# Kernel optimization log

Hardware: AMD Instinct MI355X
Metric: run time of the kernel (lower is better)

Reference implementation:

```python
import jax, jax.numpy as jnp
import numpy as np

HIDDEN = 128
NUM_RADIAL = 16
NUM_DENSE = 3
OUT_DIM = 1
N_NODES = 50000
N_EDGES = 600000


def setup_inputs() -> dict:
    key = jax.random.key(0)
    ks = jax.random.split(key, 16)
    h = jax.random.normal(ks[0], (N_NODES, HIDDEN), dtype=jnp.float32)
    radial_basis = jax.random.normal(ks[1], (N_EDGES, NUM_RADIAL), dtype=jnp.float32)
    edge_index = jax.random.randint(ks[2], (2, N_EDGES), 0, N_NODES, dtype=jnp.int32)

    def lin(k, fan_in, fan_out):
        bound = 1.0 / np.sqrt(fan_in)
        kw, kb = jax.random.split(k)
        W = jax.random.uniform(kw, (fan_in, fan_out), minval=-bound, maxval=bound, dtype=jnp.float32)
        b = jax.random.uniform(kb, (fan_out,), minval=-bound, maxval=bound, dtype=jnp.float32)
        return W, b

    rW1, rb1 = lin(ks[3], NUM_RADIAL, HIDDEN)
    rW2, rb2 = lin(ks[4], HIDDEN, HIDDEN)
    dW, db = [], []
    for i in range(NUM_DENSE):
        W, b = lin(ks[5 + i], HIDDEN, HIDDEN)
        dW.append(W); db.append(b)
    oW, ob = lin(ks[10], HIDDEN, OUT_DIM)
    return {
        "h": h, "radial_basis": radial_basis, "edge_index": edge_index,
        "rW1": rW1, "rb1": rb1, "rW2": rW2, "rb2": rb2,
        "dW0": dW[0], "db0": db[0], "dW1": dW[1], "db1": db[1], "dW2": dW[2], "db2": db[2],
        "oW": oW, "ob": ob,
    }


def reference(h, radial_basis, edge_index, rW1, rb1, rW2, rb2,
              dW0, db0, dW1, db1, dW2, db2, oW, ob):
    src, dst = edge_index[0], edge_index[1]
    # radial_net: Linear -> SiLU -> Linear, output [n_edges, hidden]
    W = jax.nn.silu(radial_basis @ rW1 + rb1) @ rW2 + rb2
    # gather -> multiply -> scatter-add (message passing)
    h_edge = h[src] * W                      # [n_edges, hidden]
    x = jax.ops.segment_sum(h_edge, dst, num_segments=h.shape[0])  # [n_atoms, hidden]
    # dense layers
    for dw, dbias in ((dW0, db0), (dW1, db1), (dW2, db2)):
        x = jax.nn.silu(x @ dw + dbias)
    return x @ oW + ob                        # [n_atoms, output_dim]
```

## Files before the change

### kernel.cpp

```cpp
#include <hip/hip_runtime.h>

typedef short bf16x8 __attribute__((ext_vector_type(8)));
typedef float f32x4 __attribute__((ext_vector_type(4)));
typedef float f32x2 __attribute__((ext_vector_type(2)));
typedef unsigned int u32x4 __attribute__((ext_vector_type(4)));

__device__ __forceinline__ unsigned short f2bf(float f) {
  unsigned int u = __float_as_uint(f);
  u = (u + 0x7FFFu + ((u >> 16) & 1u)) >> 16;
  return (unsigned short)u;
}
__device__ __forceinline__ float bf2f(unsigned short u) {
  return __uint_as_float(((unsigned int)u) << 16);
}
__device__ __forceinline__ float silu_f(float v) {
  return v * (1.0f / (1.0f + __expf(-v)));
}
__device__ __forceinline__ unsigned int pkbf(float a, float b) {
  unsigned int r;
  asm("v_cvt_pk_bf16_f32 %0, %1, %2" : "=v"(r) : "v"(a), "v"(b));
  return r;
}
__device__ __forceinline__ void st2bf(char* base, int byA, int byB, float a, float b) {
  unsigned int p = pkbf(a, b);
  *(unsigned short*)(base + byA) = (unsigned short)p;
  *(unsigned short*)(base + byB) = (unsigned short)(p >> 16);
}

__global__ void k_prep(const float* __restrict__ rW1, const float* __restrict__ rb1,
                       const float* __restrict__ rW2, const float* __restrict__ dW0,
                       const float* __restrict__ dW1, const float* __restrict__ dW2,
                       unsigned short* __restrict__ wb, int* __restrict__ hist,
                       int nzero) {
  int i = blockIdx.x * blockDim.x + threadIdx.x;
  if (i < 4096) {
    int j = i & 7, lane = (i >> 3) & 63, nt = i >> 9;
    int k = (lane >> 4) * 8 + j, n = nt * 16 + (lane & 15);
    float v = (k < 16) ? rW1[k * 128 + n] : (k == 16 ? rb1[n] : 0.0f);
    wb[i] = f2bf(v);
  } else if (i < 4096 + 4 * 16384) {
    int i2 = i - 4096, buf = i2 >> 14, r = i2 & 16383;
    int j = r & 7, lane = (r >> 3) & 63, g = r >> 9, kc = g & 3, nt = g >> 2;
    int k = kc * 32 + (lane >> 4) * 8 + j, n = nt * 16 + (lane & 15);
    const float* W = (buf == 0) ? rW2 : (buf == 1) ? dW0 : (buf == 2) ? dW1 : dW2;
    wb[4096 + buf * 16384 + r] = f2bf(W[k * 128 + n]);
  } else if (i - 69632 < nzero) {
    hist[i - 69632] = 0;
  }
}

__global__ void k_hist(const int* __restrict__ ei, int* __restrict__ hist, int E) {
  int e = blockIdx.x * blockDim.x + threadIdx.x;
  if (e < E) atomicAdd(&hist[ei[E + e]], 1);
}

__global__ __launch_bounds__(1024) void k_scanA(const int* __restrict__ hist,
                                                int* __restrict__ part, int N) {
  __shared__ int red[1024];
  const int t = threadIdx.x;
  const int i = blockIdx.x * 1024 + t;
  red[t] = (i < N) ? hist[i] : 0;
  __syncthreads();
  for (int o = 512; o; o >>= 1) {
    if (t < o) red[t] += red[t + o];
    __syncthreads();
  }
  if (t == 0) part[blockIdx.x] = red[0];
}

__global__ __launch_bounds__(1024) void k_scanC(
    const int* __restrict__ hist, const int* __restrict__ part,
    int* __restrict__ row_start, int* __restrict__ bump, int N, int nb) {
  __shared__ int sh[1024];
  __shared__ int s_off;
  const int t = threadIdx.x;
  const int b = blockIdx.x;
  if (t < 64) {
    int p = (t < nb) ? part[t] : 0;
#pragma unroll
    for (int o = 1; o < 64; o <<= 1) {
      int u = __shfl_up(p, o);
      if (t >= o) p += u;
    }
    if (b == 0) {
      if (t == 0) s_off = 0;
    } else if (t == b - 1) {
      s_off = p;
    }
  }
  __syncthreads();
  const int i = b * 1024 + t;
  const int v = (i < N) ? hist[i] : 0;
  sh[t] = v;
  __syncthreads();
  for (int o = 1; o < 1024; o <<= 1) {
    int u = (t >= o) ? sh[t - o] : 0;
    __syncthreads();
    sh[t] += u;
    __syncthreads();
  }
  const int excl = s_off + sh[t] - v;
  if (i < N) {
    row_start[i] = excl;
    bump[i] = excl;
  } else if (i == N) {
    row_start[N] = excl;
  }
}

__global__ __launch_bounds__(256, 2) void k_edge2(
    const float* __restrict__ rb, const int* __restrict__ ei,
    const float* __restrict__ h, const unsigned short* __restrict__ B1,
    const unsigned short* __restrict__ B2, const float* __restrict__ rb2,
    int* __restrict__ bump, unsigned short* __restrict__ Mbuf,
    int E, int ntiles) {
  const int lane = threadIdx.x & 63;
  const int wid = threadIdx.x >> 6;
  const int kg = lane >> 4;
  const int c15 = lane & 15;
  __shared__ __align__(16) unsigned short hid[64 * 128];

  bf16x8 b2f[8][4];
#pragma unroll
  for (int nt = 0; nt < 8; ++nt)
#pragma unroll
    for (int kc = 0; kc < 4; ++kc)
      b2f[nt][kc] = *(const bf16x8*)(B2 + (((nt * 4 + kc) * 64 + lane) << 3));

  float rb2r[8];
#pragma unroll
  for (int nt = 0; nt < 8; ++nt) rb2r[nt] = rb2[nt * 16 + c15];

  for (int t = blockIdx.x; t < ntiles; t += gridDim.x) {
    const int ebase = t * 64 + wid * 16;

    bf16x8 a1 = {};
    if (kg < 2) {
      const int e = ebase + c15;
      if (e < E) {
        const f32x4 v0 = __builtin_nontemporal_load((const f32x4*)(rb + (size_t)e * 16 + kg * 8));
        const f32x4 v1 = __builtin_nontemporal_load((const f32x4*)(rb + (size_t)e * 16 + kg * 8 + 4));
        unsigned int p0 = pkbf(v0[0], v0[1]), p1 = pkbf(v0[2], v0[3]);
        unsigned int p2 = pkbf(v1[0], v1[1]), p3 = pkbf(v1[2], v1[3]);
        a1[0] = (short)(p0 & 0xffff); a1[1] = (short)(p0 >> 16);
        a1[2] = (short)(p1 & 0xffff); a1[3] = (short)(p1 >> 16);
        a1[4] = (short)(p2 & 0xffff); a1[5] = (short)(p2 >> 16);
        a1[6] = (short)(p3 & 0xffff); a1[7] = (short)(p3 >> 16);
      }
    } else if (kg == 2) {
      a1[0] = (short)0x3F80;
    }

#pragma unroll
    for (int nt = 0; nt < 8; ++nt) {
      bf16x8 b1 = *(const bf16x8*)(B1 + ((nt * 64 + lane) << 3));
      f32x4 d1 = {};
      d1 = __builtin_amdgcn_mfma_f32_16x16x32_bf16(a1, b1, d1, 0, 0, 0);
#pragma unroll
      for (int r = 0; r < 4; r += 2) {
        const int row0 = wid * 16 + kg * 4 + r;
        const int row1 = row0 + 1;
        const int col2 = (nt * 16 + c15) * 2;
        st2bf((char*)hid,
              (row0 * 256 + col2) ^ ((row0 & 7) << 4),
              (row1 * 256 + col2) ^ ((row1 & 7) << 4),
              silu_f(d1[r]), silu_f(d1[r + 1]));
      }
    }

    const int arow = wid * 16 + c15;
    f32x4 acc[8] = {};
#pragma unroll
    for (int kc = 0; kc < 4; ++kc) {
      int byt = arow * 256 + (kc * 32 + kg * 8) * 2;
      byt ^= (arow & 7) << 4;
      const bf16x8 a2 = *(const bf16x8*)((const char*)hid + byt);
#pragma unroll
      for (int nt = 0; nt < 8; ++nt)
        acc[nt] = __builtin_amdgcn_mfma_f32_16x16x32_bf16(a2, b2f[nt][kc], acc[nt], 0, 0, 0);
    }

#pragma unroll
    for (int nt = 0; nt < 8; ++nt)
#pragma unroll
      for (int r = 0; r < 4; r += 2) {
        const int row0 = wid * 16 + kg * 4 + r;
        const int row1 = row0 + 1;
        const int col2 = (nt * 16 + c15) * 2;
        st2bf((char*)hid,
              (row0 * 256 + col2) ^ ((row0 & 7) << 4),
              (row1 * 256 + col2) ^ ((row1 & 7) << 4),
              acc[nt][r] + rb2r[nt], acc[nt][r + 1] + rb2r[nt]);
      }

#pragma unroll
    for (int pass = 0; pass < 2; ++pass) {
      const int ro = wid * 16 + pass * 8 + (lane >> 3);
      const int e = t * 64 + ro;
      if (e < E) {
        const int d = ei[E + e];
        int pc = 0;
        if ((lane & 7) == 0) pc = atomicAdd(&bump[d], 1);
        const int p = __shfl(pc, lane & 56);
        const int s = ei[e];
        const int cg = (lane & 7) * 16;
        const int swz = (ro & 7) << 4;
        const int bas = ro * 256 + cg * 2;
        const bf16x8 w0 = *(const bf16x8*)((const char*)hid + (bas ^ swz));
        const bf16x8 w1 = *(const bf16x8*)((const char*)hid + ((bas + 16) ^ swz));
        const f32x4* hp = (const f32x4*)(h + (size_t)s * 128 + cg);
        const f32x4 h0 = hp[0], h1 = hp[1], h2 = hp[2], h3 = hp[3];
        u32x4 m0, m1;
        m0[0] = pkbf(bf2f((unsigned short)w0[0]) * h0[0], bf2f((unsigned short)w0[1]) * h0[1]);
        m0[1] = pkbf(bf2f((unsigned short)w0[2]) * h0[2], bf2f((unsigned short)w0[3]) * h0[3]);
        m0[2] = pkbf(bf2f((unsigned short)w0[4]) * h1[0], bf2f((unsigned short)w0[5]) * h1[1]);
        m0[3] = pkbf(bf2f((unsigned short)w0[6]) * h1[2], bf2f((unsigned short)w0[7]) * h1[3]);
        m1[0] = pkbf(bf2f((unsigned short)w1[0]) * h2[0], bf2f((unsigned short)w1[1]) * h2[1]);
        m1[1] = pkbf(bf2f((unsigned short)w1[2]) * h2[2], bf2f((unsigned short)w1[3]) * h2[3]);
        m1[2] = pkbf(bf2f((unsigned short)w1[4]) * h3[0], bf2f((unsigned short)w1[5]) * h3[1]);
        m1[3] = pkbf(bf2f((unsigned short)w1[6]) * h3[2], bf2f((unsigned short)w1[7]) * h3[3]);
        *(u32x4*)(Mbuf + (size_t)p * 128 + cg) = m0;
        *(u32x4*)(Mbuf + (size_t)p * 128 + cg + 8) = m1;
      }
    }
  }
}

__device__ __forceinline__ void dense_silu_layer(
    unsigned short* xt, const unsigned short* __restrict__ W,
    const float* __restrict__ bias, int wid, int kg, int c15, int lane) {
  const int arow = wid * 16 + c15;
  f32x4 acc[8] = {};
#pragma unroll
  for (int kc = 0; kc < 4; ++kc) {
    int byt = arow * 256 + (kc * 32 + kg * 8) * 2;
    byt ^= (arow & 7) << 4;
    const bf16x8 a2 = *(const bf16x8*)((const char*)xt + byt);
#pragma unroll
    for (int nt = 0; nt < 8; ++nt) {
      const bf16x8 bf = *(const bf16x8*)(W + (((nt * 4 + kc) * 64 + lane) << 3));
      acc[nt] = __builtin_amdgcn_mfma_f32_16x16x32_bf16(a2, bf, acc[nt], 0, 0, 0);
    }
  }
#pragma unroll
  for (int nt = 0; nt < 8; ++nt) {
    const float b = bias[nt * 16 + c15];
#pragma unroll
    for (int r = 0; r < 4; r += 2) {
      const int row0 = wid * 16 + kg * 4 + r;
      const int row1 = row0 + 1;
      const int col2 = (nt * 16 + c15) * 2;
      st2bf((char*)xt,
            (row0 * 256 + col2) ^ ((row0 & 7) << 4),
            (row1 * 256 + col2) ^ ((row1 & 7) << 4),
            silu_f(acc[nt][r] + b), silu_f(acc[nt][r + 1] + b));
    }
  }
}

__global__ __launch_bounds__(512) void k_gtile(
    const unsigned short* __restrict__ Mbuf, const int* __restrict__ row_start,
    const unsigned short* __restrict__ Dw, const float* __restrict__ db0,
    const float* __restrict__ db1, const float* __restrict__ db2,
    const float* __restrict__ oW, const float* __restrict__ ob,
    float* __restrict__ out, int NN, int tiles) {
  const int tid = threadIdx.x;
  const int lane = tid & 63;
  const int wid = tid >> 6;
  const int kg = lane >> 4;
  const int c15 = lane & 15;
  __shared__ __align__(16) unsigned short xt[128 * 128];

  for (int t = blockIdx.x; t < tiles; t += gridDim.x) {
    if (t != (int)blockIdx.x) __syncthreads();
    const int rbase = wid * 16;
    const int nbase = t * 128 + rbase;

    for (int i = 0; i < 16; i += 4) {
      int base[4], len[4];
#pragma unroll
      for (int j = 0; j < 4; ++j) {
        const int n = nbase + i + j;
        if (n < NN) {
          const int b0 = row_start[n];
          base[j] = b0;
          len[j] = row_start[n + 1] - b0;
        } else {
          base[j] = 0;
          len[j] = 0;
        }
      }
      int maxlen = len[0] > len[1] ? len[0] : len[1];
      maxlen = maxlen > len[2] ? maxlen : len[2];
      maxlen = maxlen > len[3] ? maxlen : len[3];
      float s[4][8] = {};
      for (int off = kg; off < maxlen; off += 4) {
#pragma unroll
        for (int j = 0; j < 4; ++j) {
          if (off < len[j]) {
            const bf16x8 v = *(const bf16x8*)(Mbuf + (size_t)(base[j] + off) * 128 + c15 * 8);
#pragma unroll
            for (int k = 0; k < 8; ++k) s[j][k] += bf2f((unsigned short)v[k]);
          }
        }
      }
#pragma unroll
      for (int j = 0; j < 4; ++j)
#pragma unroll
        for (int k = 0; k < 8; ++k) {
          float v = s[j][k];
          v += __shfl_xor(v, 16);
          v += __shfl_xor(v, 32);
          s[j][k] = v;
        }
#pragma unroll
      for (int j = 0; j < 4; ++j) {
        if (kg == j) {
          const int n = nbase + i + j;
          if (n < NN) {
            const int row = rbase + i + j;
            u32x4 w;
            w[0] = pkbf(s[j][0], s[j][1]);
            w[1] = pkbf(s[j][2], s[j][3]);
            w[2] = pkbf(s[j][4], s[j][5]);
            w[3] = pkbf(s[j][6], s[j][7]);
            const int byt = (row * 256 + c15 * 16) ^ ((row & 7) << 4);
            *(u32x4*)((char*)xt + byt) = w;
          }
        }
      }
    }

    __syncthreads();

    dense_silu_layer(xt, Dw, db0, wid, kg, c15, lane);
    dense_silu_layer(xt, Dw + 16384, db1, wid, kg, c15, lane);

    {
      const int arow = wid * 16 + c15;
      const unsigned short* W = Dw + 32768;
      f32x4 acc[8] = {};
#pragma unroll
      for (int kc = 0; kc < 4; ++kc) {
        int byt = arow * 256 + (kc * 32 + kg * 8) * 2;
        byt ^= (arow & 7) << 4;
        const bf16x8 a2 = *(const bf16x8*)((const char*)xt + byt);
#pragma unroll
        for (int nt = 0; nt < 8; ++nt) {
          const bf16x8 bf = *(const bf16x8*)(W + (((nt * 4 + kc) * 64 + lane) << 3));
          acc[nt] = __builtin_amdgcn_mfma_f32_16x16x32_bf16(a2, bf, acc[nt], 0, 0, 0);
        }
      }
      const float obv = ob[0];
#pragma unroll
      for (int r = 0; r < 4; ++r) {
        float p = 0.f;
#pragma unroll
        for (int nt = 0; nt < 8; ++nt) {
          const float b = db2[nt * 16 + c15];
          p += silu_f(acc[nt][r] + b) * oW[nt * 16 + c15];
        }
        p += __shfl_xor(p, 1);
        p += __shfl_xor(p, 2);
        p += __shfl_xor(p, 4);
        p += __shfl_xor(p, 8);
        const int n = nbase + kg * 4 + r;
        if (c15 == 0 && n < NN) out[n] = p + obv;
      }
    }
  }
}

__global__ __launch_bounds__(256, 2) void k_edge(
    const float* __restrict__ rb, const int* __restrict__ ei,
    const float* __restrict__ h, const unsigned short* __restrict__ B1,
    const unsigned short* __restrict__ B2, const float* __restrict__ rb2,
    float* __restrict__ x, int E, int ntiles) {
  const int lane = threadIdx.x & 63;
  const int wid = threadIdx.x >> 6;
  const int kg = lane >> 4;
  const int c15 = lane & 15;
  __shared__ __align__(16) unsigned short hid[64 * 128];

  bf16x8 b2f[8][4];
#pragma unroll
  for (int nt = 0; nt < 8; ++nt)
#pragma unroll
    for (int kc = 0; kc < 4; ++kc)
      b2f[nt][kc] = *(const bf16x8*)(B2 + (((nt * 4 + kc) * 64 + lane) << 3));

  float rb2r[8];
#pragma unroll
  for (int nt = 0; nt < 8; ++nt) rb2r[nt] = rb2[nt * 16 + c15];

  for (int t = blockIdx.x; t < ntiles; t += gridDim.x) {
    const int ebase = t * 64 + wid * 16;
    bf16x8 a1 = {};
    if (kg < 2) {
      const int e = ebase + c15;
      if (e < E) {
        const f32x4 v0 = *(const f32x4*)(rb + (size_t)e * 16 + kg * 8);
        const f32x4 v1 = *(const f32x4*)(rb + (size_t)e * 16 + kg * 8 + 4);
        a1[0] = (short)f2bf(v0[0]); a1[1] = (short)f2bf(v0[1]);
        a1[2] = (short)f2bf(v0[2]); a1[3] = (short)f2bf(v0[3]);
        a1[4] = (short)f2bf(v1[0]); a1[5] = (short)f2bf(v1[1]);
        a1[6] = (short)f2bf(v1[2]); a1[7] = (short)f2bf(v1[3]);
      }
    } else if (kg == 2) {
      a1[0] = (short)0x3F80;
    }
#pragma unroll
    for (int nt = 0; nt < 8; ++nt) {
      bf16x8 b1 = *(const bf16x8*)(B1 + ((nt * 64 + lane) << 3));
      f32x4 d1 = {};
      d1 = __builtin_amdgcn_mfma_f32_16x16x32_bf16(a1, b1, d1, 0, 0, 0);
#pragma unroll
      for (int r = 0; r < 4; ++r) {
        const int row = wid * 16 + kg * 4 + r;
        int byt = row * 256 + (nt * 16 + c15) * 2;
        byt ^= (row & 7) << 4;
        *(unsigned short*)((char*)hid + byt) = f2bf(silu_f(d1[r]));
      }
    }
    const int arow = wid * 16 + c15;
    f32x4 acc[8] = {};
#pragma unroll
    for (int kc = 0; kc < 4; ++kc) {
      int byt = arow * 256 + (kc * 32 + kg * 8) * 2;
      byt ^= (arow & 7) << 4;
      const bf16x8 a2 = *(const bf16x8*)((const char*)hid + byt);
#pragma unroll
      for (int nt = 0; nt < 8; ++nt)
        acc[nt] = __builtin_amdgcn_mfma_f32_16x16x32_bf16(a2, b2f[nt][kc], acc[nt], 0, 0, 0);
    }
#pragma unroll
    for (int r = 0; r < 4; ++r) {
      const int e = ebase + kg * 4 + r;
      if (e < E) {
        const int s = ei[e];
        const int d = ei[E + e];
#pragma unroll
        for (int nt = 0; nt < 8; ++nt) {
          const int col = nt * 16 + c15;
          const float w = acc[nt][r] + rb2r[nt];
          const float hv = h[(size_t)s * 128 + col];
          atomicAdd(x + (size_t)d * 128 + col, w * hv);
        }
      }
    }
  }
}

__global__ __launch_bounds__(256, 2) void k_dense(
    float* __restrict__ x, const unsigned short* __restrict__ Bw,
    const float* __restrict__ bias, int M) {
  const int lane = threadIdx.x & 63;
  const int wid = threadIdx.x >> 6;
  const int kg = lane >> 4;
  const int c15 = lane & 15;

  bf16x8 bf[8][4];
#pragma unroll
  for (int nt = 0; nt < 8; ++nt)
#pragma unroll
    for (int kc = 0; kc < 4; ++kc)
      bf[nt][kc] = *(const bf16x8*)(Bw + (((nt * 4 + kc) * 64 + lane) << 3));

  float br[8];
#pragma unroll
  for (int nt = 0; nt < 8; ++nt) br[nt] = bias[nt * 16 + c15];

  const int tiles = (M + 63) >> 6;
  for (int t = blockIdx.x; t < tiles; t += gridDim.x) {
    const int rbase = t * 64 + wid * 16;
    const int row = rbase + c15;
    bf16x8 a[4];
#pragma unroll
    for (int kc = 0; kc < 4; ++kc) {
      bf16x8 az = {};
      if (row < M) {
        const f32x4 v0 = *(const f32x4*)(x + (size_t)row * 128 + kc * 32 + kg * 8);
        const f32x4 v1 = *(const f32x4*)(x + (size_t)row * 128 + kc * 32 + kg * 8 + 4);
        az[0] = (short)f2bf(v0[0]); az[1] = (short)f2bf(v0[1]);
        az[2] = (short)f2bf(v0[2]); az[3] = (short)f2bf(v0[3]);
        az[4] = (short)f2bf(v1[0]); az[5] = (short)f2bf(v1[1]);
        az[6] = (short)f2bf(v1[2]); az[7] = (short)f2bf(v1[3]);
      }
      a[kc] = az;
    }
    f32x4 acc[8] = {};
#pragma unroll
    for (int kc = 0; kc < 4; ++kc)
#pragma unroll
      for (int nt = 0; nt < 8; ++nt)
        acc[nt] = __builtin_amdgcn_mfma_f32_16x16x32_bf16(a[kc], bf[nt][kc], acc[nt], 0, 0, 0);
#pragma unroll
    for (int r = 0; r < 4; ++r) {
      const int orow = rbase + kg * 4 + r;
      if (orow < M) {
#pragma unroll
        for (int nt = 0; nt < 8; ++nt)
          x[(size_t)orow * 128 + nt * 16 + c15] = silu_f(acc[nt][r] + br[nt]);
      }
    }
  }
}

__global__ void k_out(const float* __restrict__ x, const float* __restrict__ oW,
                      const float* __restrict__ ob, float* __restrict__ out, int M) {
  const int lane = threadIdx.x & 63;
  const int w = (int)((blockIdx.x * blockDim.x + threadIdx.x) >> 6);
  const int nw = (int)((gridDim.x * blockDim.x) >> 6);
  const float w0 = oW[lane], w1 = oW[64 + lane];
  const float obv = ob[0];
  for (int row = w; row < M; row += nw) {
    float a = x[(size_t)row * 128 + lane] * w0 + x[(size_t)row * 128 + 64 + lane] * w1;
#pragma unroll
    for (int m = 32; m; m >>= 1) a += __shfl_xor(a, m);
    if (lane == 0) out[row] = a + obv;
  }
}

extern "C" void kernel_launch(void* const* d_in, const int* in_sizes, int n_in,
                              void* d_out, int out_size, void* d_ws, size_t ws_size,
                              hipStream_t stream) {
  const float* h   = (const float*)d_in[0];
  const float* rb  = (const float*)d_in[1];
  const int*   ei  = (const int*)d_in[2];
  const float* rW1 = (const float*)d_in[3];
  const float* rb1 = (const float*)d_in[4];
  const float* rW2 = (const float*)d_in[5];
  const float* rb2 = (const float*)d_in[6];
  const float* dW0 = (const float*)d_in[7];
  const float* db0 = (const float*)d_in[8];
  const float* dW1 = (const float*)d_in[9];
  const float* db1 = (const float*)d_in[10];
  const float* dW2 = (const float*)d_in[11];
  const float* db2 = (const float*)d_in[12];
  const float* oW  = (const float*)d_in[13];
  const float* ob  = (const float*)d_in[14];

  const int NN = in_sizes[0] / 128;
  const int E  = in_sizes[1] / 16;

  char* base = (char*)d_ws;
  size_t off = 0;
  auto alloc = [&](size_t bytes) {
    char* p = base + off;
    off += (bytes + 255) & ~(size_t)255;
    return p;
  };
  float* x            = (float*)alloc((size_t)NN * 128 * 4);
  unsigned short* wb  = (unsigned short*)alloc((size_t)69632 * 2);
  int* row_start      = (int*)alloc((size_t)(NN + 1) * 4);
  int* hist           = (int*)alloc((size_t)NN * 4);
  int* bump           = (int*)alloc((size_t)NN * 4);
  int* part           = (int*)alloc((size_t)64 * 4);
  unsigned short* Mb  = (unsigned short*)alloc((size_t)E * 256);
  const bool fits = off <= ws_size && NN <= 65535;

  const int ntiles = (E + 63) / 64;
  const int gE = (E + 255) / 256;
  const int nb = (NN + 1023) / 1024;

  if (fits) {
    k_prep<<<(69632 + NN + 255) / 256, 256, 0, stream>>>(rW1, rb1, rW2, dW0, dW1,
                                                         dW2, wb, hist, NN);
    k_hist<<<gE, 256, 0, stream>>>(ei, hist, E);
    k_scanA<<<nb, 1024, 0, stream>>>(hist, part, NN);
    k_scanC<<<nb, 1024, 0, stream>>>(hist, part, row_start, bump, NN, nb);
    const int eg = ntiles < 2048 ? ntiles : 2048;
    k_edge2<<<eg, 256, 0, stream>>>(rb, ei, h, wb, wb + 4096, rb2, bump, Mb, E, ntiles);
    const int gt = (NN + 127) / 128;
    k_gtile<<<gt, 512, 0, stream>>>(Mb, row_start, wb + 20480, db0, db1, db2,
                                    oW, ob, (float*)d_out, NN, gt);
  } else {
    k_prep<<<(69632 + 255) / 256, 256, 0, stream>>>(rW1, rb1, rW2, dW0, dW1,
                                                    dW2, wb, hist, 0);
    hipMemsetAsync(x, 0, (size_t)NN * 512, stream);
    const int eg = ntiles < 1024 ? ntiles : 1024;
    k_edge<<<eg, 256, 0, stream>>>(rb, ei, h, wb, wb + 4096, rb2, x, E, ntiles);
    k_dense<<<512, 256, 0, stream>>>(x, wb + 20480, db0, NN);
    k_dense<<<512, 256, 0, stream>>>(x, wb + 36864, db1, NN);
    k_dense<<<512, 256, 0, stream>>>(x, wb + 53248, db2, NN);
    k_out<<<512, 256, 0, stream>>>(x, oW, ob, (float*)d_out, NN);
  }
}
```

Before: 299.4 us.

## Write edge messages in edge order and gather them via a CSR permutation index

The edge kernel now writes each message row to its own edge slot instead of a scattered CSR position obtained by an atomic bump, which removes the per-row atomics from the edge kernel. A separate k_pos kernel builds an edge-index permutation, and the gather-tile kernel reads messages indirectly through that index. The goal is coalesced stores and an edge kernel that no longer depends on the histogram and scan. The cost is an extra kernel launch, an extra index read per message, and random-access reads of 256-byte message rows in the gather kernel.

```diff
diff --git a/kernel.cpp b/kernel.cpp
--- a/kernel.cpp
+++ b/kernel.cpp
@@ -108,12 +108,20 @@
   }
 }
 
+__global__ void k_pos(const int* __restrict__ ei, int* __restrict__ bump,
+                      int* __restrict__ eidx, int E) {
+  int e = blockIdx.x * blockDim.x + threadIdx.x;
+  if (e < E) {
+    const int p = atomicAdd(&bump[ei[E + e]], 1);
+    eidx[p] = e;
+  }
+}
+
 __global__ __launch_bounds__(256, 2) void k_edge2(
     const float* __restrict__ rb, const int* __restrict__ ei,
     const float* __restrict__ h, const unsigned short* __restrict__ B1,
     const unsigned short* __restrict__ B2, const float* __restrict__ rb2,
-    int* __restrict__ bump, unsigned short* __restrict__ Mbuf,
-    int E, int ntiles) {
+    unsigned short* __restrict__ Mbuf, int E, int ntiles) {
   const int lane = threadIdx.x & 63;
   const int wid = threadIdx.x >> 6;
   const int kg = lane >> 4;
@@ -198,10 +206,6 @@
       const int ro = wid * 16 + pass * 8 + (lane >> 3);
       const int e = t * 64 + ro;
       if (e < E) {
-        const int d = ei[E + e];
-        int pc = 0;
-        if ((lane & 7) == 0) pc = atomicAdd(&bump[d], 1);
-        const int p = __shfl(pc, lane & 56);
         const int s = ei[e];
         const int cg = (lane & 7) * 16;
         const int swz = (ro & 7) << 4;
@@ -219,8 +223,8 @@
         m1[1] = pkbf(bf2f((unsigned short)w1[2]) * h2[2], bf2f((unsigned short)w1[3]) * h2[3]);
         m1[2] = pkbf(bf2f((unsigned short)w1[4]) * h3[0], bf2f((unsigned short)w1[5]) * h3[1]);
         m1[3] = pkbf(bf2f((unsigned short)w1[6]) * h3[2], bf2f((unsigned short)w1[7]) * h3[3]);
-        *(u32x4*)(Mbuf + (size_t)p * 128 + cg) = m0;
-        *(u32x4*)(Mbuf + (size_t)p * 128 + cg + 8) = m1;
+        *(u32x4*)(Mbuf + (size_t)e * 128 + cg) = m0;
+        *(u32x4*)(Mbuf + (size_t)e * 128 + cg + 8) = m1;
       }
     }
   }
@@ -260,10 +264,10 @@
 
 __global__ __launch_bounds__(512) void k_gtile(
     const unsigned short* __restrict__ Mbuf, const int* __restrict__ row_start,
-    const unsigned short* __restrict__ Dw, const float* __restrict__ db0,
-    const float* __restrict__ db1, const float* __restrict__ db2,
-    const float* __restrict__ oW, const float* __restrict__ ob,
-    float* __restrict__ out, int NN, int tiles) {
+    const int* __restrict__ eidx, const unsigned short* __restrict__ Dw,
+    const float* __restrict__ db0, const float* __restrict__ db1,
+    const float* __restrict__ db2, const float* __restrict__ oW,
+    const float* __restrict__ ob, float* __restrict__ out, int NN, int tiles) {
   const int tid = threadIdx.x;
   const int lane = tid & 63;
   const int wid = tid >> 6;
@@ -295,13 +299,30 @@
       maxlen = maxlen > len[3] ? maxlen : len[3];
       float s[4][8] = {};
       for (int off = kg; off < maxlen; off += 4) {
-#pragma unroll
-        for (int j = 0; j < 4; ++j) {
-          if (off < len[j]) {
-            const bf16x8 v = *(const bf16x8*)(Mbuf + (size_t)(base[j] + off) * 128 + c15 * 8);
-#pragma unroll
-            for (int k = 0; k < 8; ++k) s[j][k] += bf2f((unsigned short)v[k]);
-          }
+        int r0 = 0, r1 = 0, r2 = 0, r3 = 0;
+        if (off < len[0]) r0 = eidx[base[0] + off];
+        if (off < len[1]) r1 = eidx[base[1] + off];
+        if (off < len[2]) r2 = eidx[base[2] + off];
+        if (off < len[3]) r3 = eidx[base[3] + off];
+        if (off < len[0]) {
+          const bf16x8 v = *(const bf16x8*)(Mbuf + (size_t)r0 * 128 + c15 * 8);
+#pragma unroll
+          for (int k = 0; k < 8; ++k) s[0][k] += bf2f((unsigned short)v[k]);
+        }
+        if (off < len[1]) {
+          const bf16x8 v = *(const bf16x8*)(Mbuf + (size_t)r1 * 128 + c15 * 8);
+#pragma unroll
+          for (int k = 0; k < 8; ++k) s[1][k] += bf2f((unsigned short)v[k]);
+        }
+        if (off < len[2]) {
+          const bf16x8 v = *(const bf16x8*)(Mbuf + (size_t)r2 * 128 + c15 * 8);
+#pragma unroll
+          for (int k = 0; k < 8; ++k) s[2][k] += bf2f((unsigned short)v[k]);
+        }
+        if (off < len[3]) {
+          const bf16x8 v = *(const bf16x8*)(Mbuf + (size_t)r3 * 128 + c15 * 8);
+#pragma unroll
+          for (int k = 0; k < 8; ++k) s[3][k] += bf2f((unsigned short)v[k]);
         }
       }
 #pragma unroll
@@ -556,6 +577,7 @@
   int* hist           = (int*)alloc((size_t)NN * 4);
   int* bump           = (int*)alloc((size_t)NN * 4);
   int* part           = (int*)alloc((size_t)64 * 4);
+  int* eidx           = (int*)alloc((size_t)E * 4);
   unsigned short* Mb  = (unsigned short*)alloc((size_t)E * 256);
   const bool fits = off <= ws_size && NN <= 65535;
 
@@ -566,14 +588,15 @@
   if (fits) {
     k_prep<<<(69632 + NN + 255) / 256, 256, 0, stream>>>(rW1, rb1, rW2, dW0, dW1,
                                                          dW2, wb, hist, NN);
+    const int eg = ntiles < 2048 ? ntiles : 2048;
+    k_edge2<<<eg, 256, 0, stream>>>(rb, ei, h, wb, wb + 4096, rb2, Mb, E, ntiles);
     k_hist<<<gE, 256, 0, stream>>>(ei, hist, E);
     k_scanA<<<nb, 1024, 0, stream>>>(hist, part, NN);
     k_scanC<<<nb, 1024, 0, stream>>>(hist, part, row_start, bump, NN, nb);
-    const int eg = ntiles < 2048 ? ntiles : 2048;
-    k_edge2<<<eg, 256, 0, stream>>>(rb, ei, h, wb, wb + 4096, rb2, bump, Mb, E, ntiles);
+    k_pos<<<gE, 256, 0, stream>>>(ei, bump, eidx, E);
     const int gt = (NN + 127) / 128;
-    k_gtile<<<gt, 512, 0, stream>>>(Mb, row_start, wb + 20480, db0, db1, db2,
-                                    oW, ob, (float*)d_out, NN, gt);
+    k_gtile<<<gt, 512, 0, stream>>>(Mb, row_start, eidx, wb + 20480, db0, db1,
+                                    db2, oW, ob, (float*)d_out, NN, gt);
   } else {
     k_prep<<<(69632 + 255) / 256, 256, 0, stream>>>(rW1, rb1, rW2, dW0, dW1,
                                                     dW2, wb, hist, 0);
```

Result: slower. 340.5 us (+13.7%).
